# Kernel tuning notes

Measured on AMD Instinct MI355X. Metric: run time of the kernel, lower is better.

Reference implementation:

```python
import jax, jax.numpy as jnp
import numpy as np

N_NODES = 50000
N_EDGES = 800000
IN_DIM, HIDDEN, OUT_DIM, HEADS = 64, 32, 32, 4
NEG_SLOPE = 0.2  # PyG GATConv default negative_slope


def _glorot(key, shape):
    fan = shape[0] + shape[-1]
    lim = jnp.sqrt(6.0 / fan)
    return jax.random.uniform(key, shape, jnp.float32, -lim, lim)


def setup_inputs() -> dict:
    key = jax.random.key(0)
    ks = jax.random.split(key, 8)
    x = jax.random.normal(ks[0], (N_NODES, IN_DIM), jnp.float32)
    edge_index = jax.random.randint(ks[1], (2, N_EDGES), 0, N_NODES, jnp.int64)
    return {
        "x": x,
        "edge_index": edge_index,
        "W1": _glorot(ks[2], (IN_DIM, HEADS * HIDDEN)),
        "att_src1": _glorot(ks[3], (HEADS, HIDDEN)),
        "att_dst1": _glorot(ks[4], (HEADS, HIDDEN)),
        "b1": jnp.zeros((HEADS * HIDDEN,), jnp.float32),
        "W2": _glorot(ks[5], (HEADS * HIDDEN, OUT_DIM)),
        "att_src2": _glorot(ks[6], (1, OUT_DIM)),
        "att_dst2": _glorot(ks[7], (1, OUT_DIM)),
        "b2": jnp.zeros((OUT_DIM,), jnp.float32),
    }


def gat_conv(x, src, dst, W, att_src, att_dst, bias, concat):
    # PyG GATConv: linear per head, edge attention, segment softmax over dst, scatter-add.
    N = x.shape[0]
    heads, out = att_src.shape
    h = (x @ W).reshape(N, heads, out)                       # (N, H, O)
    a_s = jnp.einsum('nho,ho->nh', h, att_src)               # (N, H)
    a_d = jnp.einsum('nho,ho->nh', h, att_dst)
    e = jax.nn.leaky_relu(a_s[src] + a_d[dst], NEG_SLOPE)    # (E, H)
    # numerically-stable segment softmax over incoming edges of each dst node
    emax = jax.ops.segment_max(e, dst, num_segments=N)       # (N, H)
    ex = jnp.exp(e - emax[dst])
    denom = jax.ops.segment_sum(ex, dst, num_segments=N)
    alpha = ex / denom[dst]                                  # (E, H)
    msg = h[src] * alpha[:, :, None]                         # (E, H, O) gather + weight
    agg = jax.ops.segment_sum(msg, dst, num_segments=N)      # (N, H, O) scatter-add
    outp = agg.reshape(N, heads * out) if concat else agg.mean(axis=1)
    return outp + bias


def reference(x, edge_index, W1, att_src1, att_dst1, b1, W2, att_src2, att_dst2, b2):
    N = x.shape[0]
    # PyG GATConv adds self-loops by default
    loops = jnp.arange(N, dtype=edge_index.dtype)
    src = jnp.concatenate([edge_index[0], loops])
    dst = jnp.concatenate([edge_index[1], loops])
    h = gat_conv(x, src, dst, W1, att_src1, att_dst1, b1, concat=True)
    h = jax.nn.elu(h)
    return gat_conv(h, src, dst, W2, att_src2, att_dst2, b2, concat=False)
```

## Files before the change

### kernel.cpp

```cpp
#include <hip/hip_runtime.h>
#include <hip/hip_bf16.h>
#include <math.h>

#define N_NODES 50000
#define N_EDGES 800000
#define E_TOT   (N_EDGES + N_NODES)
#define NEG_SLOPE 0.2f
#define SLOT_CAP 64
#define GEMM_BLOCKS ((N_NODES + 63) / 64)
#define BUCKET_BLOCKS ((E_TOT + 255) / 256)

__device__ __forceinline__ float lrelu(float x) { return x >= 0.f ? x : NEG_SLOPE * x; }
__device__ __forceinline__ float frcp(float x) { return __builtin_amdgcn_rcpf(x); }

__device__ __forceinline__ unsigned bf16r(float x) {
    unsigned u = __float_as_uint(x);
    return (u + 0x7fffu + ((u >> 16) & 1u)) >> 16;
}
__device__ __forceinline__ unsigned pack2(float lo, float hi) {
    return bf16r(lo) | (bf16r(hi) << 16);
}
__device__ __forceinline__ float bflo(unsigned u) { return __uint_as_float(u << 16); }
__device__ __forceinline__ float bfhi(unsigned u) { return __uint_as_float(u & 0xffff0000u); }

__global__ __launch_bounds__(256) void
gemm1_bucket(const float* __restrict__ x, const float* __restrict__ W1,
             const float* __restrict__ att_s, const float* __restrict__ att_d,
             unsigned* __restrict__ h1u, float* __restrict__ as1,
             float* __restrict__ ad1,
             const int* __restrict__ ei, int* __restrict__ cnt,
             int* __restrict__ slot) {
    int b = blockIdx.x;
    if (b >= GEMM_BLOCKS) {
        int e = (b - GEMM_BLOCKS) * 256 + threadIdx.x;
        if (e < E_TOT) {
            int s, d;
            if (e < N_EDGES) { s = ei[e]; d = ei[N_EDGES + e]; }
            else             { s = d = e - N_EDGES; }
            int pos = atomicAdd(&cnt[d], 1);
            if (pos < SLOT_CAP) slot[(size_t)pos * N_NODES + d] = s;
        }
        return;
    }
    int t = threadIdx.x;
    int w = __builtin_amdgcn_readfirstlane(t >> 6);
    int l = t & 63;
    int nbase = b * 64;

    __shared__ float xs[64][65];

    const float4* xv = (const float4*)(x + (size_t)nbase * 64);
    int nvalid = min(64, N_NODES - nbase);
    for (int i = t; i < nvalid * 16; i += 256) {
        float4 v = xv[i];
        int n = i >> 4, k4 = (i & 15) * 4;
        xs[n][k4] = v.x; xs[n][k4 + 1] = v.y; xs[n][k4 + 2] = v.z; xs[n][k4 + 3] = v.w;
    }
    __syncthreads();

    float acc[32];
#pragma unroll
    for (int e = 0; e < 32; ++e) acc[e] = 0.f;

#pragma unroll 4
    for (int k = 0; k < 64; ++k) {
        float xk = xs[l][k];
        const float4* wr = (const float4*)(W1 + k * 128 + w * 32);
#pragma unroll
        for (int e4 = 0; e4 < 8; ++e4) {
            float4 wv = wr[e4];
            acc[e4 * 4 + 0] += xk * wv.x;
            acc[e4 * 4 + 1] += xk * wv.y;
            acc[e4 * 4 + 2] += xk * wv.z;
            acc[e4 * 4 + 3] += xk * wv.w;
        }
    }

    int n = nbase + l;
    if (n < N_NODES) {
        uint4* hv = (uint4*)(h1u + (size_t)n * 64 + w * 16);
#pragma unroll
        for (int e4 = 0; e4 < 4; ++e4) {
            uint4 pk;
            pk.x = pack2(acc[e4 * 8 + 0], acc[e4 * 8 + 1]);
            pk.y = pack2(acc[e4 * 8 + 2], acc[e4 * 8 + 3]);
            pk.z = pack2(acc[e4 * 8 + 4], acc[e4 * 8 + 5]);
            pk.w = pack2(acc[e4 * 8 + 6], acc[e4 * 8 + 7]);
            hv[e4] = pk;
        }
        float ps = 0.f, pd = 0.f;
#pragma unroll
        for (int e = 0; e < 32; ++e) {
            ps += acc[e] * att_s[w * 32 + e];
            pd += acc[e] * att_d[w * 32 + e];
        }
        as1[n * 4 + w] = ps;
        ad1[n * 4 + w] = pd;
    }
}

__global__ void node_agg1(const int* __restrict__ cnt, const int* __restrict__ slot,
                          const float* __restrict__ as1, const float* __restrict__ ad1,
                          const uint4* __restrict__ h1q, const float* __restrict__ b1,
                          const float* __restrict__ W2, const float* __restrict__ att_s2,
                          const float* __restrict__ att_d2,
                          unsigned* __restrict__ h2u, float* __restrict__ as2,
                          float* __restrict__ ad2) {
    int tb = threadIdx.x;
    int wv = tb >> 6, t = tb & 63;
    int n = blockIdx.x * 2 + wv;
    int deg = min(cnt[n], SLOT_CAP);
    float4 ad = *(const float4*)(ad1 + n * 4);

    __shared__ float els[2][SLOT_CAP * 4];
    __shared__ int  slds[2][SLOT_CAP];
    __shared__ float hrow[2][128];

    {
        int ah = t & 3;
        float adh = (ah == 0) ? ad.x : (ah == 1) ? ad.y : (ah == 2) ? ad.z : ad.w;
        for (int p = (t >> 2); p < deg; p += 16) {
            int s = slot[(size_t)p * N_NODES + n];
            els[wv][p * 4 + ah] = __expf(lrelu(as1[s * 4 + ah] + adh));
            if (ah == 0) slds[wv][p] = s;
        }
    }
    __syncthreads();

    int oct = t & 15, g = t >> 4, hq = oct >> 2;
    float a0 = 0.f, a1 = 0.f, a2 = 0.f, a3 = 0.f;
    float a4 = 0.f, a5 = 0.f, a6 = 0.f, a7 = 0.f;
    float accE = 0.f;
#pragma unroll 2
    for (int p = g; p < deg; p += 8) {
        float exA = els[wv][p * 4 + hq];
        uint4 hvA = h1q[(size_t)slds[wv][p] * 16 + oct];
        int pB = p + 4;
        float exB = 0.f;
        uint4 hvB = make_uint4(0u, 0u, 0u, 0u);
        if (pB < deg) {
            exB = els[wv][pB * 4 + hq];
            hvB = h1q[(size_t)slds[wv][pB] * 16 + oct];
        }
        accE += exA + exB;
        a0 += exA * bflo(hvA.x) + exB * bflo(hvB.x);
        a1 += exA * bfhi(hvA.x) + exB * bfhi(hvB.x);
        a2 += exA * bflo(hvA.y) + exB * bflo(hvB.y);
        a3 += exA * bfhi(hvA.y) + exB * bfhi(hvB.y);
        a4 += exA * bflo(hvA.z) + exB * bflo(hvB.z);
        a5 += exA * bfhi(hvA.z) + exB * bfhi(hvB.z);
        a6 += exA * bflo(hvA.w) + exB * bflo(hvB.w);
        a7 += exA * bfhi(hvA.w) + exB * bfhi(hvB.w);
    }
    for (int m = 16; m <= 32; m <<= 1) {
        a0 += __shfl_xor(a0, m, 64); a1 += __shfl_xor(a1, m, 64);
        a2 += __shfl_xor(a2, m, 64); a3 += __shfl_xor(a3, m, 64);
        a4 += __shfl_xor(a4, m, 64); a5 += __shfl_xor(a5, m, 64);
        a6 += __shfl_xor(a6, m, 64); a7 += __shfl_xor(a7, m, 64);
        accE += __shfl_xor(accE, m, 64);
    }
    {
        float rE = frcp(accE);
        const float4* b1v = (const float4*)b1;
        float4 bA = b1v[oct * 2], bB = b1v[oct * 2 + 1];
        float v0 = a0 * rE + bA.x, v1 = a1 * rE + bA.y;
        float v2 = a2 * rE + bA.z, v3 = a3 * rE + bA.w;
        float v4 = a4 * rE + bB.x, v5 = a5 * rE + bB.y;
        float v6 = a6 * rE + bB.z, v7 = a7 * rE + bB.w;
        v0 = v0 > 0.f ? v0 : __expf(v0) - 1.f;
        v1 = v1 > 0.f ? v1 : __expf(v1) - 1.f;
        v2 = v2 > 0.f ? v2 : __expf(v2) - 1.f;
        v3 = v3 > 0.f ? v3 : __expf(v3) - 1.f;
        v4 = v4 > 0.f ? v4 : __expf(v4) - 1.f;
        v5 = v5 > 0.f ? v5 : __expf(v5) - 1.f;
        v6 = v6 > 0.f ? v6 : __expf(v6) - 1.f;
        v7 = v7 > 0.f ? v7 : __expf(v7) - 1.f;
        if (g == 0) {
            float4* hw = (float4*)&hrow[wv][oct * 8];
            hw[0] = make_float4(v0, v1, v2, v3);
            hw[1] = make_float4(v4, v5, v6, v7);
        }
    }
    __syncthreads();

    {
        int l = t & 31, half = t >> 5;
        const float* hr = hrow[wv];
        int k0 = half * 64;
        float pacc = 0.f;
#pragma unroll 16
        for (int k = 0; k < 64; ++k)
            pacc += hr[k0 + k] * W2[(k0 + k) * 32 + l];
        pacc += __shfl_xor(pacc, 32, 64);
        float hv2 = pacc;
        float ps = hv2 * att_s2[l];
        float pd = hv2 * att_d2[l];
        for (int m = 16; m >= 1; m >>= 1) {
            ps += __shfl_xor(ps, m, 64);
            pd += __shfl_xor(pd, m, 64);
        }
        if (t == 0) { as2[n] = ps; ad2[n] = pd; }
        float hvn = __shfl_down(hv2, 1, 64);
        if (t < 32 && (t & 1) == 0)
            h2u[n * 16 + (t >> 1)] = pack2(hv2, hvn);
    }
}

__global__ void node_agg2(const int* __restrict__ cnt, const int* __restrict__ slot,
                          const float* __restrict__ as2, const float* __restrict__ ad2,
                          const uint2* __restrict__ h2d, const float* __restrict__ b2,
                          float* __restrict__ out) {
    int n = blockIdx.x;
    int t = threadIdx.x;
    int c = t & 7, g = t >> 3;
    int deg = min(cnt[n], SLOT_CAP);
    float ad = ad2[n];

    __shared__ float els[SLOT_CAP];
    __shared__ int  slds[SLOT_CAP];

    if (t < deg) {
        int s = slot[(size_t)t * N_NODES + n];
        els[t] = __expf(lrelu(as2[s] + ad));
        slds[t] = s;
    }
    __syncthreads();

    float a0 = 0.f, a1 = 0.f, a2 = 0.f, a3 = 0.f;
    float accE = 0.f;
    for (int p = g; p < deg; p += 16) {
        float exA = els[p];
        uint2 hvA = h2d[(size_t)slds[p] * 8 + c];
        int pB = p + 8;
        float exB = 0.f;
        uint2 hvB = make_uint2(0u, 0u);
        if (pB < deg) {
            exB = els[pB];
            hvB = h2d[(size_t)slds[pB] * 8 + c];
        }
        accE += exA + exB;
        a0 += exA * bflo(hvA.x) + exB * bflo(hvB.x);
        a1 += exA * bfhi(hvA.x) + exB * bfhi(hvB.x);
        a2 += exA * bflo(hvA.y) + exB * bflo(hvB.y);
        a3 += exA * bfhi(hvA.y) + exB * bfhi(hvB.y);
    }
    for (int m = 8; m <= 32; m <<= 1) {
        a0 += __shfl_xor(a0, m, 64); a1 += __shfl_xor(a1, m, 64);
        a2 += __shfl_xor(a2, m, 64); a3 += __shfl_xor(a3, m, 64);
        accE += __shfl_xor(accE, m, 64);
    }
    if (t < 8) {
        float rE = frcp(accE);
        const float4* bb = (const float4*)(b2 + t * 4);
        float4 r = make_float4(a0 * rE + bb->x, a1 * rE + bb->y,
                               a2 * rE + bb->z, a3 * rE + bb->w);
        *(float4*)(out + n * 32 + t * 4) = r;
    }
}

extern "C" void kernel_launch(void* const* d_in, const int* in_sizes, int n_in,
                              void* d_out, int out_size, void* d_ws, size_t ws_size,
                              hipStream_t stream) {
    const float* x        = (const float*)d_in[0];
    const int*   ei       = (const int*)d_in[1];
    const float* W1       = (const float*)d_in[2];
    const float* att_src1 = (const float*)d_in[3];
    const float* att_dst1 = (const float*)d_in[4];
    const float* b1       = (const float*)d_in[5];
    const float* W2       = (const float*)d_in[6];
    const float* att_src2 = (const float*)d_in[7];
    const float* att_dst2 = (const float*)d_in[8];
    const float* b2       = (const float*)d_in[9];
    float* out = (float*)d_out;

    float* p = (float*)d_ws;
    unsigned* h1u = (unsigned*)p; p += N_NODES * 64;
    unsigned* h2u = (unsigned*)p; p += N_NODES * 16;
    float* as1   = p; p += N_NODES * 4;
    float* ad1   = p; p += N_NODES * 4;
    float* as2   = p; p += N_NODES;
    float* ad2   = p; p += N_NODES;
    int* ip = (int*)p;
    int* cnt   = ip; ip += N_NODES;
    int* slot  = ip; ip += N_NODES * SLOT_CAP;

    hipMemsetAsync(cnt, 0, N_NODES * sizeof(int), stream);

    gemm1_bucket<<<GEMM_BLOCKS + BUCKET_BLOCKS, 256, 0, stream>>>(
        x, W1, att_src1, att_dst1, h1u, as1, ad1, ei, cnt, slot);

    node_agg1<<<N_NODES / 2, 128, 0, stream>>>(cnt, slot, as1, ad1,
                                               (const uint4*)h1u, b1,
                                               W2, att_src2, att_dst2, h2u, as2, ad2);

    node_agg2<<<N_NODES, 64, 0, stream>>>(cnt, slot, as2, ad2,
                                          (const uint2*)h2u, b2, out);
}
```

Baseline: 137.4 us.

## Interleave slot table in groups of four and pack four nodes per agg2 block

Changes the per-node neighbor slot table from position-major layout to groups of four consecutive positions per node, so a node's neighbor list is read from fewer cache lines. Also packs four nodes (one per wavefront) into each node_agg2 block instead of one node per 64-thread block, reducing block count and scheduling overhead. The layout shift spreads the scatter writes differently and adds a block-wide barrier shared across four independent nodes.

```diff
diff --git a/kernel.cpp b/kernel.cpp
--- a/kernel.cpp
+++ b/kernel.cpp
@@ -7,11 +7,16 @@
 #define E_TOT   (N_EDGES + N_NODES)
 #define NEG_SLOPE 0.2f
 #define SLOT_CAP 64
+#define N4 ((size_t)N_NODES * 4)
 #define GEMM_BLOCKS ((N_NODES + 63) / 64)
 #define BUCKET_BLOCKS ((E_TOT + 255) / 256)
 
 __device__ __forceinline__ float lrelu(float x) { return x >= 0.f ? x : NEG_SLOPE * x; }
 __device__ __forceinline__ float frcp(float x) { return __builtin_amdgcn_rcpf(x); }
+
+__device__ __forceinline__ size_t slot_idx(int pos, int n) {
+    return (size_t)(pos >> 2) * N4 + (size_t)n * 4 + (pos & 3);
+}
 
 __device__ __forceinline__ unsigned bf16r(float x) {
     unsigned u = __float_as_uint(x);
@@ -38,7 +43,7 @@
             if (e < N_EDGES) { s = ei[e]; d = ei[N_EDGES + e]; }
             else             { s = d = e - N_EDGES; }
             int pos = atomicAdd(&cnt[d], 1);
-            if (pos < SLOT_CAP) slot[(size_t)pos * N_NODES + d] = s;
+            if (pos < SLOT_CAP) slot[slot_idx(pos, d)] = s;
         }
         return;
     }
@@ -120,7 +125,7 @@
         int ah = t & 3;
         float adh = (ah == 0) ? ad.x : (ah == 1) ? ad.y : (ah == 2) ? ad.z : ad.w;
         for (int p = (t >> 2); p < deg; p += 16) {
-            int s = slot[(size_t)p * N_NODES + n];
+            int s = slot[slot_idx(p, n)];
             els[wv][p * 4 + ah] = __expf(lrelu(as1[s * 4 + ah] + adh));
             if (ah == 0) slds[wv][p] = s;
         }
@@ -206,37 +211,40 @@
     }
 }
 
-__global__ void node_agg2(const int* __restrict__ cnt, const int* __restrict__ slot,
-                          const float* __restrict__ as2, const float* __restrict__ ad2,
-                          const uint2* __restrict__ h2d, const float* __restrict__ b2,
-                          float* __restrict__ out) {
-    int n = blockIdx.x;
-    int t = threadIdx.x;
+__global__ __launch_bounds__(256) void
+node_agg2(const int* __restrict__ cnt, const int* __restrict__ slot,
+          const float* __restrict__ as2, const float* __restrict__ ad2,
+          const uint2* __restrict__ h2d, const float* __restrict__ b2,
+          float* __restrict__ out) {
+    int tb = threadIdx.x;
+    int wv = tb >> 6, t = tb & 63;
+    int n = blockIdx.x * 4 + wv;
+    if (n >= N_NODES) return;
     int c = t & 7, g = t >> 3;
     int deg = min(cnt[n], SLOT_CAP);
     float ad = ad2[n];
 
-    __shared__ float els[SLOT_CAP];
-    __shared__ int  slds[SLOT_CAP];
+    __shared__ float els[4][SLOT_CAP];
+    __shared__ int  slds[4][SLOT_CAP];
 
     if (t < deg) {
-        int s = slot[(size_t)t * N_NODES + n];
-        els[t] = __expf(lrelu(as2[s] + ad));
-        slds[t] = s;
+        int s = slot[slot_idx(t, n)];
+        els[wv][t] = __expf(lrelu(as2[s] + ad));
+        slds[wv][t] = s;
     }
     __syncthreads();
 
     float a0 = 0.f, a1 = 0.f, a2 = 0.f, a3 = 0.f;
     float accE = 0.f;
     for (int p = g; p < deg; p += 16) {
-        float exA = els[p];
-        uint2 hvA = h2d[(size_t)slds[p] * 8 + c];
+        float exA = els[wv][p];
+        uint2 hvA = h2d[(size_t)slds[wv][p] * 8 + c];
         int pB = p + 8;
         float exB = 0.f;
         uint2 hvB = make_uint2(0u, 0u);
         if (pB < deg) {
-            exB = els[pB];
-            hvB = h2d[(size_t)slds[pB] * 8 + c];
+            exB = els[wv][pB];
+            hvB = h2d[(size_t)slds[wv][pB] * 8 + c];
         }
         accE += exA + exB;
         a0 += exA * bflo(hvA.x) + exB * bflo(hvB.x);
@@ -293,6 +301,6 @@
                                                (const uint4*)h1u, b1,
                                                W2, att_src2, att_dst2, h2u, as2, ad2);
 
-    node_agg2<<<N_NODES, 64, 0, stream>>>(cnt, slot, as2, ad2,
-                                          (const uint2*)h2u, b2, out);
-}
+    node_agg2<<<(N_NODES + 3) / 4, 256, 0, stream>>>(cnt, slot, as2, ad2,
+                                                     (const uint2*)h2u, b2, out);
+}
```

After: 139.0 us. No clear change (+1.1%).

## Aggregate raw bf16 inputs before the layer-1 projection and interleave slot layout

Applied to the files above, without the earlier changes.

Uses linearity to reorder layer 1: attention scores come from folded W1·att vectors, and each node aggregates the 64-dim bf16 input features per head instead of gathering the 128-dim projected h1. The W1 projection then runs per node after aggregation, which halves the gathered bytes per edge and removes the h1 store. The slot table is also re-laid out so each node's first four slots are contiguous, which improves locality when reading a node's neighbour list. The cost is extra per-node matmul work in node_agg1 (64x128 per node) and more accumulator registers.

```diff
diff --git a/kernel.cpp b/kernel.cpp
--- a/kernel.cpp
+++ b/kernel.cpp
@@ -7,11 +7,16 @@
 #define E_TOT   (N_EDGES + N_NODES)
 #define NEG_SLOPE 0.2f
 #define SLOT_CAP 64
+#define N4 ((size_t)N_NODES * 4)
 #define GEMM_BLOCKS ((N_NODES + 63) / 64)
 #define BUCKET_BLOCKS ((E_TOT + 255) / 256)
 
 __device__ __forceinline__ float lrelu(float x) { return x >= 0.f ? x : NEG_SLOPE * x; }
 __device__ __forceinline__ float frcp(float x) { return __builtin_amdgcn_rcpf(x); }
+
+__device__ __forceinline__ size_t slot_idx(int pos, int n) {
+    return (size_t)(pos >> 2) * N4 + (size_t)n * 4 + (pos & 3);
+}
 
 __device__ __forceinline__ unsigned bf16r(float x) {
     unsigned u = __float_as_uint(x);
@@ -24,12 +29,11 @@
 __device__ __forceinline__ float bfhi(unsigned u) { return __uint_as_float(u & 0xffff0000u); }
 
 __global__ __launch_bounds__(256) void
-gemm1_bucket(const float* __restrict__ x, const float* __restrict__ W1,
-             const float* __restrict__ att_s, const float* __restrict__ att_d,
-             unsigned* __restrict__ h1u, float* __restrict__ as1,
-             float* __restrict__ ad1,
-             const int* __restrict__ ei, int* __restrict__ cnt,
-             int* __restrict__ slot) {
+prep_bucket(const float* __restrict__ x, const float* __restrict__ W1,
+            const float* __restrict__ att_s, const float* __restrict__ att_d,
+            uint2* __restrict__ xb, float* __restrict__ as1, float* __restrict__ ad1,
+            const int* __restrict__ ei, int* __restrict__ cnt,
+            int* __restrict__ slot) {
     int b = blockIdx.x;
     if (b >= GEMM_BLOCKS) {
         int e = (b - GEMM_BLOCKS) * 256 + threadIdx.x;
@@ -38,70 +42,68 @@
             if (e < N_EDGES) { s = ei[e]; d = ei[N_EDGES + e]; }
             else             { s = d = e - N_EDGES; }
             int pos = atomicAdd(&cnt[d], 1);
-            if (pos < SLOT_CAP) slot[(size_t)pos * N_NODES + d] = s;
+            if (pos < SLOT_CAP) slot[slot_idx(pos, d)] = s;
         }
         return;
     }
     int t = threadIdx.x;
-    int w = __builtin_amdgcn_readfirstlane(t >> 6);
-    int l = t & 63;
     int nbase = b * 64;
+    int nvalid = min(64, N_NODES - nbase);
 
     __shared__ float xs[64][65];
+    __shared__ float wsL[64][4], wdL[64][4];
 
     const float4* xv = (const float4*)(x + (size_t)nbase * 64);
-    int nvalid = min(64, N_NODES - nbase);
     for (int i = t; i < nvalid * 16; i += 256) {
         float4 v = xv[i];
         int n = i >> 4, k4 = (i & 15) * 4;
         xs[n][k4] = v.x; xs[n][k4 + 1] = v.y; xs[n][k4 + 2] = v.z; xs[n][k4 + 3] = v.w;
     }
-    __syncthreads();
-
-    float acc[32];
-#pragma unroll
-    for (int e = 0; e < 32; ++e) acc[e] = 0.f;
-
-#pragma unroll 4
-    for (int k = 0; k < 64; ++k) {
-        float xk = xs[l][k];
-        const float4* wr = (const float4*)(W1 + k * 128 + w * 32);
-#pragma unroll
-        for (int e4 = 0; e4 < 8; ++e4) {
-            float4 wv = wr[e4];
-            acc[e4 * 4 + 0] += xk * wv.x;
-            acc[e4 * 4 + 1] += xk * wv.y;
-            acc[e4 * 4 + 2] += xk * wv.z;
-            acc[e4 * 4 + 3] += xk * wv.w;
-        }
-    }
-
-    int n = nbase + l;
-    if (n < N_NODES) {
-        uint4* hv = (uint4*)(h1u + (size_t)n * 64 + w * 16);
-#pragma unroll
-        for (int e4 = 0; e4 < 4; ++e4) {
-            uint4 pk;
-            pk.x = pack2(acc[e4 * 8 + 0], acc[e4 * 8 + 1]);
-            pk.y = pack2(acc[e4 * 8 + 2], acc[e4 * 8 + 3]);
-            pk.z = pack2(acc[e4 * 8 + 4], acc[e4 * 8 + 5]);
-            pk.w = pack2(acc[e4 * 8 + 6], acc[e4 * 8 + 7]);
-            hv[e4] = pk;
-        }
-        float ps = 0.f, pd = 0.f;
-#pragma unroll
-        for (int e = 0; e < 32; ++e) {
-            ps += acc[e] * att_s[w * 32 + e];
-            pd += acc[e] * att_d[w * 32 + e];
-        }
-        as1[n * 4 + w] = ps;
-        ad1[n * 4 + w] = pd;
+    {
+        int k = t >> 2, h = t & 3;
+        float s = 0.f, d = 0.f;
+        const float* wr = W1 + k * 128 + h * 32;
+        const float* asr = att_s + h * 32;
+        const float* adr = att_d + h * 32;
+#pragma unroll 8
+        for (int j = 0; j < 32; ++j) {
+            float w = wr[j];
+            s += w * asr[j];
+            d += w * adr[j];
+        }
+        wsL[k][h] = s; wdL[k][h] = d;
+    }
+    __syncthreads();
+
+    for (int i = t; i < nvalid * 16; i += 256) {
+        int n = i >> 4, o = i & 15;
+        uint2 v;
+        v.x = pack2(xs[n][o * 4 + 0], xs[n][o * 4 + 1]);
+        v.y = pack2(xs[n][o * 4 + 2], xs[n][o * 4 + 3]);
+        xb[(size_t)(nbase + n) * 16 + o] = v;
+    }
+
+    {
+        int l = t & 63, h = t >> 6;
+        if (l < nvalid) {
+            float ps = 0.f, pd = 0.f;
+#pragma unroll 8
+            for (int k = 0; k < 64; ++k) {
+                float xk = xs[l][k];
+                ps += xk * wsL[k][h];
+                pd += xk * wdL[k][h];
+            }
+            int n = nbase + l;
+            as1[n * 4 + h] = ps;
+            ad1[n * 4 + h] = pd;
+        }
     }
 }
 
 __global__ void node_agg1(const int* __restrict__ cnt, const int* __restrict__ slot,
                           const float* __restrict__ as1, const float* __restrict__ ad1,
-                          const uint4* __restrict__ h1q, const float* __restrict__ b1,
+                          const uint2* __restrict__ xb, const float* __restrict__ b1,
+                          const float* __restrict__ W1,
                           const float* __restrict__ W2, const float* __restrict__ att_s2,
                           const float* __restrict__ att_d2,
                           unsigned* __restrict__ h2u, float* __restrict__ as2,
@@ -112,74 +114,93 @@
     int deg = min(cnt[n], SLOT_CAP);
     float4 ad = *(const float4*)(ad1 + n * 4);
 
-    __shared__ float els[2][SLOT_CAP * 4];
-    __shared__ int  slds[2][SLOT_CAP];
+    __shared__ float4 els4[2][SLOT_CAP];
+    __shared__ int   slds[2][SLOT_CAP];
+    __shared__ float xaggL[2][4][64];
     __shared__ float hrow[2][128];
 
     {
+        float* elsf = (float*)&els4[wv][0];
         int ah = t & 3;
         float adh = (ah == 0) ? ad.x : (ah == 1) ? ad.y : (ah == 2) ? ad.z : ad.w;
         for (int p = (t >> 2); p < deg; p += 16) {
-            int s = slot[(size_t)p * N_NODES + n];
-            els[wv][p * 4 + ah] = __expf(lrelu(as1[s * 4 + ah] + adh));
+            int s = slot[slot_idx(p, n)];
+            elsf[p * 4 + ah] = __expf(lrelu(as1[s * 4 + ah] + adh));
             if (ah == 0) slds[wv][p] = s;
         }
     }
     __syncthreads();
 
-    int oct = t & 15, g = t >> 4, hq = oct >> 2;
-    float a0 = 0.f, a1 = 0.f, a2 = 0.f, a3 = 0.f;
-    float a4 = 0.f, a5 = 0.f, a6 = 0.f, a7 = 0.f;
-    float accE = 0.f;
-#pragma unroll 2
+    int oct = t & 15, g = t >> 4;
+    float4 aH0 = {0,0,0,0}, aH1 = {0,0,0,0}, aH2 = {0,0,0,0}, aH3 = {0,0,0,0};
+    float4 accE = {0,0,0,0};
     for (int p = g; p < deg; p += 8) {
-        float exA = els[wv][p * 4 + hq];
-        uint4 hvA = h1q[(size_t)slds[wv][p] * 16 + oct];
+        float4 exA = els4[wv][p];
+        uint2 vA = xb[(size_t)slds[wv][p] * 16 + oct];
         int pB = p + 4;
-        float exB = 0.f;
-        uint4 hvB = make_uint4(0u, 0u, 0u, 0u);
+        float4 exB = {0,0,0,0};
+        uint2 vB = make_uint2(0u, 0u);
         if (pB < deg) {
-            exB = els[wv][pB * 4 + hq];
-            hvB = h1q[(size_t)slds[wv][pB] * 16 + oct];
-        }
-        accE += exA + exB;
-        a0 += exA * bflo(hvA.x) + exB * bflo(hvB.x);
-        a1 += exA * bfhi(hvA.x) + exB * bfhi(hvB.x);
-        a2 += exA * bflo(hvA.y) + exB * bflo(hvB.y);
-        a3 += exA * bfhi(hvA.y) + exB * bfhi(hvB.y);
-        a4 += exA * bflo(hvA.z) + exB * bflo(hvB.z);
-        a5 += exA * bfhi(hvA.z) + exB * bfhi(hvB.z);
-        a6 += exA * bflo(hvA.w) + exB * bflo(hvB.w);
-        a7 += exA * bfhi(hvA.w) + exB * bfhi(hvB.w);
+            exB = els4[wv][pB];
+            vB = xb[(size_t)slds[wv][pB] * 16 + oct];
+        }
+        float x0A = bflo(vA.x), x1A = bfhi(vA.x), x2A = bflo(vA.y), x3A = bfhi(vA.y);
+        float x0B = bflo(vB.x), x1B = bfhi(vB.x), x2B = bflo(vB.y), x3B = bfhi(vB.y);
+        accE.x += exA.x + exB.x; accE.y += exA.y + exB.y;
+        accE.z += exA.z + exB.z; accE.w += exA.w + exB.w;
+        aH0.x += exA.x * x0A + exB.x * x0B; aH0.y += exA.x * x1A + exB.x * x1B;
+        aH0.z += exA.x * x2A + exB.x * x2B; aH0.w += exA.x * x3A + exB.x * x3B;
+        aH1.x += exA.y * x0A + exB.y * x0B; aH1.y += exA.y * x1A + exB.y * x1B;
+        aH1.z += exA.y * x2A + exB.y * x2B; aH1.w += exA.y * x3A + exB.y * x3B;
+        aH2.x += exA.z * x0A + exB.z * x0B; aH2.y += exA.z * x1A + exB.z * x1B;
+        aH2.z += exA.z * x2A + exB.z * x2B; aH2.w += exA.z * x3A + exB.z * x3B;
+        aH3.x += exA.w * x0A + exB.w * x0B; aH3.y += exA.w * x1A + exB.w * x1B;
+        aH3.z += exA.w * x2A + exB.w * x2B; aH3.w += exA.w * x3A + exB.w * x3B;
     }
     for (int m = 16; m <= 32; m <<= 1) {
-        a0 += __shfl_xor(a0, m, 64); a1 += __shfl_xor(a1, m, 64);
-        a2 += __shfl_xor(a2, m, 64); a3 += __shfl_xor(a3, m, 64);
-        a4 += __shfl_xor(a4, m, 64); a5 += __shfl_xor(a5, m, 64);
-        a6 += __shfl_xor(a6, m, 64); a7 += __shfl_xor(a7, m, 64);
-        accE += __shfl_xor(accE, m, 64);
-    }
-    {
-        float rE = frcp(accE);
-        const float4* b1v = (const float4*)b1;
-        float4 bA = b1v[oct * 2], bB = b1v[oct * 2 + 1];
-        float v0 = a0 * rE + bA.x, v1 = a1 * rE + bA.y;
-        float v2 = a2 * rE + bA.z, v3 = a3 * rE + bA.w;
-        float v4 = a4 * rE + bB.x, v5 = a5 * rE + bB.y;
-        float v6 = a6 * rE + bB.z, v7 = a7 * rE + bB.w;
+        aH0.x += __shfl_xor(aH0.x, m, 64); aH0.y += __shfl_xor(aH0.y, m, 64);
+        aH0.z += __shfl_xor(aH0.z, m, 64); aH0.w += __shfl_xor(aH0.w, m, 64);
+        aH1.x += __shfl_xor(aH1.x, m, 64); aH1.y += __shfl_xor(aH1.y, m, 64);
+        aH1.z += __shfl_xor(aH1.z, m, 64); aH1.w += __shfl_xor(aH1.w, m, 64);
+        aH2.x += __shfl_xor(aH2.x, m, 64); aH2.y += __shfl_xor(aH2.y, m, 64);
+        aH2.z += __shfl_xor(aH2.z, m, 64); aH2.w += __shfl_xor(aH2.w, m, 64);
+        aH3.x += __shfl_xor(aH3.x, m, 64); aH3.y += __shfl_xor(aH3.y, m, 64);
+        aH3.z += __shfl_xor(aH3.z, m, 64); aH3.w += __shfl_xor(aH3.w, m, 64);
+        accE.x += __shfl_xor(accE.x, m, 64); accE.y += __shfl_xor(accE.y, m, 64);
+        accE.z += __shfl_xor(accE.z, m, 64); accE.w += __shfl_xor(accE.w, m, 64);
+    }
+    if (g == 0) {
+        float r0 = frcp(accE.x), r1 = frcp(accE.y), r2 = frcp(accE.z), r3 = frcp(accE.w);
+        float4* q0 = (float4*)&xaggL[wv][0][oct * 4];
+        float4* q1 = (float4*)&xaggL[wv][1][oct * 4];
+        float4* q2 = (float4*)&xaggL[wv][2][oct * 4];
+        float4* q3 = (float4*)&xaggL[wv][3][oct * 4];
+        *q0 = make_float4(aH0.x * r0, aH0.y * r0, aH0.z * r0, aH0.w * r0);
+        *q1 = make_float4(aH1.x * r1, aH1.y * r1, aH1.z * r1, aH1.w * r1);
+        *q2 = make_float4(aH2.x * r2, aH2.y * r2, aH2.z * r2, aH2.w * r2);
+        *q3 = make_float4(aH3.x * r3, aH3.y * r3, aH3.z * r3, aH3.w * r3);
+    }
+    __syncthreads();
+
+    {
+        int d0 = t, d1 = t + 64;
+        int h0 = t >> 5;
+        const float* xa0 = xaggL[wv][h0];
+        const float* xa1 = xaggL[wv][2 + h0];
+        float acc0 = 0.f, acc1 = 0.f;
+#pragma unroll 8
+        for (int k = 0; k < 64; ++k) {
+            float w0 = W1[k * 128 + d0];
+            float w1 = W1[k * 128 + d1];
+            acc0 += xa0[k] * w0;
+            acc1 += xa1[k] * w1;
+        }
+        float v0 = acc0 + b1[d0];
+        float v1 = acc1 + b1[d1];
         v0 = v0 > 0.f ? v0 : __expf(v0) - 1.f;
         v1 = v1 > 0.f ? v1 : __expf(v1) - 1.f;
-        v2 = v2 > 0.f ? v2 : __expf(v2) - 1.f;
-        v3 = v3 > 0.f ? v3 : __expf(v3) - 1.f;
-        v4 = v4 > 0.f ? v4 : __expf(v4) - 1.f;
-        v5 = v5 > 0.f ? v5 : __expf(v5) - 1.f;
-        v6 = v6 > 0.f ? v6 : __expf(v6) - 1.f;
-        v7 = v7 > 0.f ? v7 : __expf(v7) - 1.f;
-        if (g == 0) {
-            float4* hw = (float4*)&hrow[wv][oct * 8];
-            hw[0] = make_float4(v0, v1, v2, v3);
-            hw[1] = make_float4(v4, v5, v6, v7);
-        }
+        hrow[wv][d0] = v0;
+        hrow[wv][d1] = v1;
     }
     __syncthreads();
 
@@ -220,7 +241,7 @@
     __shared__ int  slds[SLOT_CAP];
 
     if (t < deg) {
-        int s = slot[(size_t)t * N_NODES + n];
+        int s = slot[slot_idx(t, n)];
         els[t] = __expf(lrelu(as2[s] + ad));
         slds[t] = s;
     }
@@ -274,7 +295,7 @@
     float* out = (float*)d_out;
 
     float* p = (float*)d_ws;
-    unsigned* h1u = (unsigned*)p; p += N_NODES * 64;
+    uint2* xb = (uint2*)p;        p += N_NODES * 32;
     unsigned* h2u = (unsigned*)p; p += N_NODES * 16;
     float* as1   = p; p += N_NODES * 4;
     float* ad1   = p; p += N_NODES * 4;
@@ -286,11 +307,11 @@
 
     hipMemsetAsync(cnt, 0, N_NODES * sizeof(int), stream);
 
-    gemm1_bucket<<<GEMM_BLOCKS + BUCKET_BLOCKS, 256, 0, stream>>>(
-        x, W1, att_src1, att_dst1, h1u, as1, ad1, ei, cnt, slot);
+    prep_bucket<<<GEMM_BLOCKS + BUCKET_BLOCKS, 256, 0, stream>>>(
+        x, W1, att_src1, att_dst1, xb, as1, ad1, ei, cnt, slot);
 
     node_agg1<<<N_NODES / 2, 128, 0, stream>>>(cnt, slot, as1, ad1,
-                                               (const uint4*)h1u, b1,
+                                               xb, b1, W1,
                                                W2, att_src2, att_dst2, h2u, as2, ad2);
 
     node_agg2<<<N_NODES, 64, 0, stream>>>(cnt, slot, as2, ad2,
```

New measurement: 170.5 us. 1.24x slower.
